# Performance work log

Hardware: AMD Instinct MI355X
Metric: run time of the kernel (lower is better)

Reference implementation:

```python
import jax, jax.numpy as jnp
import numpy as np

EMBED_DIM = 1024
FFN_DIM = 4096
N_QUBITS = 10


def setup_inputs() -> dict:
    key = jax.random.key(0)
    k_x, k_phi, k_w1, k_w2 = jax.random.split(key, 4)
    x = jax.random.normal(k_x, (8, 2048, EMBED_DIM), dtype=jnp.float32)
    # trainable RY angles, one per wire (torchquantum init ~ U(0, 2pi); any init works for a reference)
    ry_params = jax.random.uniform(k_phi, (N_QUBITS,), dtype=jnp.float32, minval=0.0, maxval=2.0 * np.pi)
    # nn.Linear(n_qubits, ffn_dim, bias=False): weight [ffn_dim, n_qubits]
    w1 = jax.random.normal(k_w1, (FFN_DIM, N_QUBITS), dtype=jnp.float32) / np.sqrt(N_QUBITS)
    # nn.Linear(ffn_dim, embed_dim, bias=False): weight [embed_dim, ffn_dim]
    w2 = jax.random.normal(k_w2, (EMBED_DIM, FFN_DIM), dtype=jnp.float32) / np.sqrt(FFN_DIM)
    return {"x": x, "ry_params": ry_params, "w1": w1, "w2": w2}


def reference(x, ry_params, w1, w2):
    # Quantum layer in closed form: wires are unentangled.
    # |0> --RX(x_i)--RY(phi_i)--> <Z_i> = cos(x_i) * cos(phi_i)
    # Only the first N_QUBITS features of each token are encoded.
    q_out = jnp.cos(x[..., :N_QUBITS]) * jnp.cos(ry_params)  # [B, S, nq]
    # dropout is identity in eval mode
    h = jnp.einsum('bsq,fq->bsf', q_out, w1)  # [B, S, ffn]
    h = jax.nn.relu(h)
    return jnp.einsum('bsf,ef->bse', h, w2)  # [B, S, embed]
```

## Files before the change

### kernel.cpp

```cpp
#include <hip/hip_runtime.h>
#include <stdint.h>

#define M_TOK   16384
#define EMBED   1024
#define FFN     4096
#define NQ      10

#define GK 4096
#define GN 1024
#define BK 64
#define NT (GK / BK)

typedef __attribute__((ext_vector_type(8))) short  bf16x8;
typedef __attribute__((ext_vector_type(4))) float  f32x4;
typedef __attribute__((ext_vector_type(8))) unsigned short u16x8;

static __device__ __forceinline__ unsigned short f2bf(float f) {
    union { float f; unsigned u; } v; v.f = f;
    unsigned r = v.u + 0x7FFF + ((v.u >> 16) & 1);
    return (unsigned short)(r >> 16);
}

__global__ __launch_bounds__(256) void prep_w1(
    const float* __restrict__ w1, const float* __restrict__ ry,
    float* __restrict__ w1cT)
{
    __shared__ float cry[16];
    if (threadIdx.x < NQ) cry[threadIdx.x] = cosf(ry[threadIdx.x]);
    __syncthreads();
    const int f = blockIdx.x * 256 + threadIdx.x;
#pragma unroll
    for (int i = 0; i < NQ; ++i)
        w1cT[i * FFN + f] = w1[f * NQ + i] * cry[i];
}

__global__ __launch_bounds__(256) void compute_h(
    const float* __restrict__ x, const float* __restrict__ w1cT,
    unsigned short* __restrict__ h)
{
    __shared__ float cq[32 * 16];

    const int tid = threadIdx.x;
    const int t0  = blockIdx.x * 32;
    const int fb  = blockIdx.y * 2048 + tid * 8;

    for (int idx = tid; idx < 32 * NQ; idx += 256) {
        int t = idx / NQ;
        int i = idx - t * NQ;
        cq[t * 16 + i] = cosf(x[(size_t)(t0 + t) * EMBED + i]);
    }
    __syncthreads();

    float wf[8][NQ];
#pragma unroll
    for (int i = 0; i < NQ; ++i) {
        const float4 lo = *(const float4*)(w1cT + (size_t)i * FFN + fb);
        const float4 hi = *(const float4*)(w1cT + (size_t)i * FFN + fb + 4);
        wf[0][i] = lo.x; wf[1][i] = lo.y; wf[2][i] = lo.z; wf[3][i] = lo.w;
        wf[4][i] = hi.x; wf[5][i] = hi.y; wf[6][i] = hi.z; wf[7][i] = hi.w;
    }

    for (int t = 0; t < 32; ++t) {
        const float4 c0 = *(const float4*)&cq[t * 16 + 0];
        const float4 c1 = *(const float4*)&cq[t * 16 + 4];
        const float2 c2 = *(const float2*)&cq[t * 16 + 8];
        u16x8 v;
#pragma unroll
        for (int fi = 0; fi < 8; ++fi) {
            float s = c0.x * wf[fi][0] + c0.y * wf[fi][1] + c0.z * wf[fi][2]
                    + c0.w * wf[fi][3] + c1.x * wf[fi][4] + c1.y * wf[fi][5]
                    + c1.z * wf[fi][6] + c1.w * wf[fi][7] + c2.x * wf[fi][8]
                    + c2.y * wf[fi][9];
            v[fi] = f2bf(fmaxf(s, 0.f));
        }
        *(u16x8*)(h + (size_t)(t0 + t) * FFN + fb) = v;
    }
}

__global__ __launch_bounds__(256) void conv_w2(
    const float* __restrict__ w2, unsigned short* __restrict__ o)
{
    const int idx = (blockIdx.x * 256 + threadIdx.x) * 8;
    float4 a = *(const float4*)(w2 + idx);
    float4 b = *(const float4*)(w2 + idx + 4);
    u16x8 v;
    v[0] = f2bf(a.x); v[1] = f2bf(a.y); v[2] = f2bf(a.z); v[3] = f2bf(a.w);
    v[4] = f2bf(b.x); v[5] = f2bf(b.y); v[6] = f2bf(b.z); v[7] = f2bf(b.w);
    *(u16x8*)(o + idx) = v;
}

#define GL2LDS(g, l) \
    __builtin_amdgcn_global_load_lds( \
        (const __attribute__((address_space(1))) void*)(g), \
        (__attribute__((address_space(3))) void*)(l), 16, 0, 0)

__global__ __launch_bounds__(512, 2) void gemm_bt(
    const unsigned short* __restrict__ A,
    const unsigned short* __restrict__ B,
    float* __restrict__ C)
{
    __shared__ __align__(16) unsigned short As[2][256 * BK];
    __shared__ __align__(16) unsigned short Bs[2][256 * BK];

    const int tid  = threadIdx.x;
    const int wv   = tid >> 6;
    const int lane = tid & 63;
    const int wm   = wv >> 2;
    const int wn   = wv & 3;

    const int bid = blockIdx.x;
    const int wg  = (bid & 7) * 32 + (bid >> 3);
    const int m0  = (wg >> 2) * 256;
    const int n0  = (wg & 3) * 256;

    const int srow8 = lane >> 3;
    const int schk  = (lane & 7) ^ srow8;
    const char* ag = (const char*)A +
        ((size_t)(m0 + wv * 16 + srow8) * GK + schk * 8) * 2;
    const char* bg = (const char*)B +
        ((size_t)(n0 + wv * 16 + srow8) * GK + schk * 8) * 2;
    const size_t ROW8 = (size_t)8 * GK * 2;
    const size_t HALF = (size_t)128 * GK * 2;

#define STAGE_A(buf, half, ko) do { \
    GL2LDS(ag + (ko) + (half) * HALF,        (char*)As[buf] + ((half) * 128 + wv * 16) * 128); \
    GL2LDS(ag + (ko) + (half) * HALF + ROW8, (char*)As[buf] + ((half) * 128 + wv * 16 + 8) * 128); \
} while (0)
#define STAGE_B(buf, half, ko) do { \
    GL2LDS(bg + (ko) + (half) * HALF,        (char*)Bs[buf] + ((half) * 128 + wv * 16) * 128); \
    GL2LDS(bg + (ko) + (half) * HALF + ROW8, (char*)Bs[buf] + ((half) * 128 + wv * 16 + 8) * 128); \
} while (0)

    const int rr  = lane & 15;
    const int fsw = lane & 7;
    const int cc  = lane >> 4;
#define CHOFF(s) ((((s) * 4 + cc) ^ fsw) * 16)
#define AFRAG(mh, i, s) (*(const bf16x8*)(At + (wm * 128 + (mh) * 64 + (i) * 16 + rr) * 128 + CHOFF(s)))
#define BFRAG(nh, j, s) (*(const bf16x8*)(Bt + (wn * 64 + (nh) * 32 + (j) * 16 + rr) * 128 + CHOFF(s)))

    f32x4 acc[8][4] = {};

    STAGE_A(0, 0, 0); STAGE_A(0, 1, 0);
    STAGE_B(0, 0, 0); STAGE_B(0, 1, 0);
    asm volatile("s_waitcnt vmcnt(0)" ::: "memory");
    __builtin_amdgcn_s_barrier();

#pragma unroll 1
    for (int T = 0; T < NT; ++T) {
        const char* At = (const char*)As[T & 1];
        const char* Bt = (const char*)Bs[T & 1];
        const int nb   = (T + 1) & 1;
        const size_t ko = (size_t)(T + 1) * 128;
        const bool st  = (T + 1 < NT);

        bf16x8 afr[2][4];
        bf16x8 b0r[2][2];
        bf16x8 b1r[2][2];

#pragma unroll
        for (int s = 0; s < 2; ++s) {
#pragma unroll
            for (int j = 0; j < 2; ++j) b0r[s][j] = BFRAG(0, j, s);
#pragma unroll
            for (int i = 0; i < 4; ++i) afr[s][i] = AFRAG(0, i, s);
        }
        if (st) { STAGE_A(nb, 0, ko); STAGE_A(nb, 1, ko); }
        __builtin_amdgcn_s_barrier();
        asm volatile("s_waitcnt lgkmcnt(0)" ::: "memory");
        __builtin_amdgcn_sched_barrier(0);
        __builtin_amdgcn_s_setprio(1);
#pragma unroll
        for (int s = 0; s < 2; ++s)
#pragma unroll
            for (int i = 0; i < 4; ++i)
#pragma unroll
                for (int j = 0; j < 2; ++j)
                    acc[i][j] = __builtin_amdgcn_mfma_f32_16x16x32_bf16(
                        afr[s][i], b0r[s][j], acc[i][j], 0, 0, 0);
        __builtin_amdgcn_s_setprio(0);
        __builtin_amdgcn_s_barrier();

#pragma unroll
        for (int s = 0; s < 2; ++s)
#pragma unroll
            for (int j = 0; j < 2; ++j) b1r[s][j] = BFRAG(1, j, s);
        if (st) { STAGE_B(nb, 0, ko); STAGE_B(nb, 1, ko); }
        __builtin_amdgcn_s_barrier();
        asm volatile("s_waitcnt lgkmcnt(0)" ::: "memory");
        __builtin_amdgcn_sched_barrier(0);
        __builtin_amdgcn_s_setprio(1);
#pragma unroll
        for (int s = 0; s < 2; ++s)
#pragma unroll
            for (int i = 0; i < 4; ++i)
#pragma unroll
                for (int j = 0; j < 2; ++j)
                    acc[i][2 + j] = __builtin_amdgcn_mfma_f32_16x16x32_bf16(
                        afr[s][i], b1r[s][j], acc[i][2 + j], 0, 0, 0);
        __builtin_amdgcn_s_setprio(0);
        __builtin_amdgcn_s_barrier();

#pragma unroll
        for (int s = 0; s < 2; ++s)
#pragma unroll
            for (int i = 0; i < 4; ++i) afr[s][i] = AFRAG(1, i, s);
        __builtin_amdgcn_s_barrier();
        asm volatile("s_waitcnt lgkmcnt(0)" ::: "memory");
        __builtin_amdgcn_sched_barrier(0);
        __builtin_amdgcn_s_setprio(1);
#pragma unroll
        for (int s = 0; s < 2; ++s)
#pragma unroll
            for (int i = 0; i < 4; ++i)
#pragma unroll
                for (int j = 0; j < 2; ++j)
                    acc[4 + i][2 + j] = __builtin_amdgcn_mfma_f32_16x16x32_bf16(
                        afr[s][i], b1r[s][j], acc[4 + i][2 + j], 0, 0, 0);
        __builtin_amdgcn_s_setprio(0);
        __builtin_amdgcn_s_barrier();

        __builtin_amdgcn_s_setprio(1);
#pragma unroll
        for (int s = 0; s < 2; ++s)
#pragma unroll
            for (int i = 0; i < 4; ++i)
#pragma unroll
                for (int j = 0; j < 2; ++j)
                    acc[4 + i][j] = __builtin_amdgcn_mfma_f32_16x16x32_bf16(
                        afr[s][i], b0r[s][j], acc[4 + i][j], 0, 0, 0);
        __builtin_amdgcn_s_setprio(0);
        asm volatile("s_waitcnt vmcnt(0)" ::: "memory");
        __builtin_amdgcn_s_barrier();
    }

    const int cn = lane & 15;
    const int rb = (lane >> 4) * 4;
#pragma unroll
    for (int i = 0; i < 8; ++i)
#pragma unroll
        for (int j = 0; j < 4; ++j)
#pragma unroll
            for (int r = 0; r < 4; ++r) {
                const int m = m0 + wm * 128 + i * 16 + rb + r;
                const int n = n0 + wn * 64 + j * 16 + cn;
                C[(size_t)m * GN + n] = acc[i][j][r];
            }
}

extern "C" void kernel_launch(void* const* d_in, const int* in_sizes, int n_in,
                              void* d_out, int out_size, void* d_ws, size_t ws_size,
                              hipStream_t stream) {
    const float* x  = (const float*)d_in[0];
    const float* ry = (const float*)d_in[1];
    const float* w1 = (const float*)d_in[2];
    const float* w2 = (const float*)d_in[3];
    float* out = (float*)d_out;

    unsigned short* h   = (unsigned short*)d_ws;
    unsigned short* w2b = (unsigned short*)((char*)d_ws +
                           (size_t)M_TOK * FFN * sizeof(unsigned short));
    float* w1cT = (float*)w2b;

    prep_w1<<<dim3(FFN / 256), 256, 0, stream>>>(w1, ry, w1cT);
    compute_h<<<dim3(512, 2), 256, 0, stream>>>(x, w1cT, h);
    conv_w2<<<dim3((EMBED * FFN) / (256 * 8)), 256, 0, stream>>>(w2, w2b);
    gemm_bt<<<dim3(256), 512, 0, stream>>>(h, w2b, out);
}
```

Measured before the change: 268.1 us.

## Restructure GEMM main loop into a two-tile-ahead, register-prefetched software pipeline

The bf16 GEMM main loop now stages two K-tiles into LDS before starting and refills a buffer as soon as it has been consumed, so each global load has about a full tile of compute to hide behind. The next tile's first A and B fragments are read into registers before the last MFMA block of the current tile, and B fragment registers ping-pong across an unrolled pair of tiles. Most of the per-quadrant barriers and explicit lgkmcnt waits are removed. This is meant to cut barrier and LDS-latency stalls between MFMA groups, at the cost of more live registers and reliance on compiler-inserted waits for LDS reads.

```diff
diff --git a/kernel.cpp b/kernel.cpp
--- a/kernel.cpp
+++ b/kernel.cpp
@@ -130,107 +130,86 @@
     GL2LDS(bg + (ko) + (half) * HALF,        (char*)Bs[buf] + ((half) * 128 + wv * 16) * 128); \
     GL2LDS(bg + (ko) + (half) * HALF + ROW8, (char*)Bs[buf] + ((half) * 128 + wv * 16 + 8) * 128); \
 } while (0)
+#define STAGE_ALL(buf, ko) do { \
+    STAGE_A(buf, 0, ko); STAGE_A(buf, 1, ko); \
+    STAGE_B(buf, 0, ko); STAGE_B(buf, 1, ko); \
+} while (0)
 
     const int rr  = lane & 15;
     const int fsw = lane & 7;
     const int cc  = lane >> 4;
 #define CHOFF(s) ((((s) * 4 + cc) ^ fsw) * 16)
-#define AFRAG(mh, i, s) (*(const bf16x8*)(At + (wm * 128 + (mh) * 64 + (i) * 16 + rr) * 128 + CHOFF(s)))
-#define BFRAG(nh, j, s) (*(const bf16x8*)(Bt + (wn * 64 + (nh) * 32 + (j) * 16 + rr) * 128 + CHOFF(s)))
+#define RD_A(dst, Pt, mh) do { \
+    _Pragma("unroll") \
+    for (int s_ = 0; s_ < 2; ++s_) \
+        _Pragma("unroll") \
+        for (int i_ = 0; i_ < 4; ++i_) \
+            dst[s_][i_] = *(const bf16x8*)((Pt) + \
+                (wm * 128 + (mh) * 64 + i_ * 16 + rr) * 128 + CHOFF(s_)); \
+} while (0)
+#define RD_B(dst, Pt, nh) do { \
+    _Pragma("unroll") \
+    for (int s_ = 0; s_ < 2; ++s_) \
+        _Pragma("unroll") \
+        for (int j_ = 0; j_ < 2; ++j_) \
+            dst[s_][j_] = *(const bf16x8*)((Pt) + \
+                (wn * 64 + (nh) * 32 + j_ * 16 + rr) * 128 + CHOFF(s_)); \
+} while (0)
 
     f32x4 acc[8][4] = {};
 
-    STAGE_A(0, 0, 0); STAGE_A(0, 1, 0);
-    STAGE_B(0, 0, 0); STAGE_B(0, 1, 0);
-    asm volatile("s_waitcnt vmcnt(0)" ::: "memory");
+#define MFMA16(AF, BF, I0, J0) do { \
+    __builtin_amdgcn_s_setprio(1); \
+    _Pragma("unroll") \
+    for (int s_ = 0; s_ < 2; ++s_) \
+        _Pragma("unroll") \
+        for (int i_ = 0; i_ < 4; ++i_) \
+            _Pragma("unroll") \
+            for (int j_ = 0; j_ < 2; ++j_) \
+                acc[(I0) + i_][(J0) + j_] = __builtin_amdgcn_mfma_f32_16x16x32_bf16( \
+                    AF[s_][i_], BF[s_][j_], acc[(I0) + i_][(J0) + j_], 0, 0, 0); \
+    __builtin_amdgcn_s_setprio(0); \
+} while (0)
+
+    bf16x8 aA[2][4], aB[2][4], bP[2][2], bQ[2][2];
+
+    STAGE_ALL(0, 0);
+    STAGE_ALL(1, 128);
+    asm volatile("s_waitcnt vmcnt(8)" ::: "memory");
     __builtin_amdgcn_s_barrier();
+    RD_A(aA, (const char*)As[0], 0);
+    RD_B(bP, (const char*)Bs[0], 0);
+
+#define TILE(T, cur, nxt, BPm, BQm, doRead, doStage, ko2) do { \
+    const char* At = (const char*)As[cur]; \
+    const char* Bt = (const char*)Bs[cur]; \
+     \
+    RD_B(BQm, Bt, 1); \
+    MFMA16(aA, BPm, 0, 0); \
+     \
+    RD_A(aB, At, 1); \
+    MFMA16(aA, BQm, 0, 2); \
+     \
+    MFMA16(aB, BQm, 4, 2); \
+    asm volatile("s_waitcnt vmcnt(0)" ::: "memory"); \
+    __builtin_amdgcn_s_barrier(); \
+    __builtin_amdgcn_sched_barrier(0); \
+     \
+    if (doRead) { \
+        const char* An = (const char*)As[nxt]; \
+        const char* Bn = (const char*)Bs[nxt]; \
+        RD_A(aA, An, 0); \
+        RD_B(BQm, Bn, 0); \
+    } \
+    if (doStage) STAGE_ALL(cur, ko2); \
+    MFMA16(aB, BPm, 4, 0); \
+} while (0)
 
 #pragma unroll 1
-    for (int T = 0; T < NT; ++T) {
-        const char* At = (const char*)As[T & 1];
-        const char* Bt = (const char*)Bs[T & 1];
-        const int nb   = (T + 1) & 1;
-        const size_t ko = (size_t)(T + 1) * 128;
-        const bool st  = (T + 1 < NT);
-
-        bf16x8 afr[2][4];
-        bf16x8 b0r[2][2];
-        bf16x8 b1r[2][2];
-
-#pragma unroll
-        for (int s = 0; s < 2; ++s) {
-#pragma unroll
-            for (int j = 0; j < 2; ++j) b0r[s][j] = BFRAG(0, j, s);
-#pragma unroll
-            for (int i = 0; i < 4; ++i) afr[s][i] = AFRAG(0, i, s);
-        }
-        if (st) { STAGE_A(nb, 0, ko); STAGE_A(nb, 1, ko); }
-        __builtin_amdgcn_s_barrier();
-        asm volatile("s_waitcnt lgkmcnt(0)" ::: "memory");
-        __builtin_amdgcn_sched_barrier(0);
-        __builtin_amdgcn_s_setprio(1);
-#pragma unroll
-        for (int s = 0; s < 2; ++s)
-#pragma unroll
-            for (int i = 0; i < 4; ++i)
-#pragma unroll
-                for (int j = 0; j < 2; ++j)
-                    acc[i][j] = __builtin_amdgcn_mfma_f32_16x16x32_bf16(
-                        afr[s][i], b0r[s][j], acc[i][j], 0, 0, 0);
-        __builtin_amdgcn_s_setprio(0);
-        __builtin_amdgcn_s_barrier();
-
-#pragma unroll
-        for (int s = 0; s < 2; ++s)
-#pragma unroll
-            for (int j = 0; j < 2; ++j) b1r[s][j] = BFRAG(1, j, s);
-        if (st) { STAGE_B(nb, 0, ko); STAGE_B(nb, 1, ko); }
-        __builtin_amdgcn_s_barrier();
-        asm volatile("s_waitcnt lgkmcnt(0)" ::: "memory");
-        __builtin_amdgcn_sched_barrier(0);
-        __builtin_amdgcn_s_setprio(1);
-#pragma unroll
-        for (int s = 0; s < 2; ++s)
-#pragma unroll
-            for (int i = 0; i < 4; ++i)
-#pragma unroll
-                for (int j = 0; j < 2; ++j)
-                    acc[i][2 + j] = __builtin_amdgcn_mfma_f32_16x16x32_bf16(
-                        afr[s][i], b1r[s][j], acc[i][2 + j], 0, 0, 0);
-        __builtin_amdgcn_s_setprio(0);
-        __builtin_amdgcn_s_barrier();
-
-#pragma unroll
-        for (int s = 0; s < 2; ++s)
-#pragma unroll
-            for (int i = 0; i < 4; ++i) afr[s][i] = AFRAG(1, i, s);
-        __builtin_amdgcn_s_barrier();
-        asm volatile("s_waitcnt lgkmcnt(0)" ::: "memory");
-        __builtin_amdgcn_sched_barrier(0);
-        __builtin_amdgcn_s_setprio(1);
-#pragma unroll
-        for (int s = 0; s < 2; ++s)
-#pragma unroll
-            for (int i = 0; i < 4; ++i)
-#pragma unroll
-                for (int j = 0; j < 2; ++j)
-                    acc[4 + i][2 + j] = __builtin_amdgcn_mfma_f32_16x16x32_bf16(
-                        afr[s][i], b1r[s][j], acc[4 + i][2 + j], 0, 0, 0);
-        __builtin_amdgcn_s_setprio(0);
-        __builtin_amdgcn_s_barrier();
-
-        __builtin_amdgcn_s_setprio(1);
-#pragma unroll
-        for (int s = 0; s < 2; ++s)
-#pragma unroll
-            for (int i = 0; i < 4; ++i)
-#pragma unroll
-                for (int j = 0; j < 2; ++j)
-                    acc[4 + i][j] = __builtin_amdgcn_mfma_f32_16x16x32_bf16(
-                        afr[s][i], b0r[s][j], acc[4 + i][j], 0, 0, 0);
-        __builtin_amdgcn_s_setprio(0);
-        asm volatile("s_waitcnt vmcnt(0)" ::: "memory");
-        __builtin_amdgcn_s_barrier();
+    for (int tt = 0; tt < NT / 2; ++tt) {
+        const bool nl = (tt < NT / 2 - 1);
+        TILE(2 * tt, 0, 1, bP, bQ, true, nl, (size_t)(2 * tt + 2) * 128);
+        TILE(2 * tt + 1, 1, 0, bQ, bP, nl, nl, (size_t)(2 * tt + 3) * 128);
     }
 
     const int cn = lane & 15;
```

Result: faster. 255.5 us (-4.7%).
